# Kernel optimization log

Measured on AMD Instinct MI355X. Metric: run time of the kernel, lower is better.

The kernel has to match this reference:

```python
import jax, jax.numpy as jnp
import numpy as np
from jax import lax

B, C, H, W = 16, 3, 256, 256
K = 3          # lbp kernel size (odd)
POOL = 3       # avg pool size (odd so shapes are preserved)
Q = 8          # quant_len


def _build_lbp_kernel():
    mid = K // 2
    idx_pairs = [((0, 0), (K - 1, K - 1)), ((0, mid), (K - 1, mid)),
                 ((0, K - 1), (K - 1, 0)), ((mid, K - 1), (mid, 0))]
    ks = []
    for a, b in idx_pairs:
        for pos in (a, b):
            k = np.zeros((C, K, K), np.float32)
            k[:, mid, mid] = 1.0
            k[:, pos[0], pos[1]] = -1.0
            ks.append(k)
    return jnp.asarray(np.stack(ks))  # [8, C, K, K]

LBP_KERNEL = _build_lbp_kernel()
# cartesian_prod(arange(Q), arange(Q)) -> first coord slowest (row-major)
IDXS = jnp.asarray(np.stack(np.meshgrid(np.arange(Q), np.arange(Q), indexing='ij'), -1)
                   .reshape(Q * Q, 2).astype(np.float32))  # [64, 2]


def _forward(x, w_expand, b_expand, w_conv, b_conv, w_final, b_final, clamp_low, clamp_high):
    b = x.shape[0]
    # avg_pool2d(kernel=POOL, stride=1, pad=POOL//2, count_include_pad=True)
    p = POOL // 2
    xp = jnp.pad(x, ((0, 0), (0, 0), (p, p), (p, p)))
    x = lax.reduce_window(xp, 0.0, lax.add, (1, 1, POOL, POOL), (1, 1, 1, 1), 'VALID') / (POOL * POOL)
    # 8-channel LBP difference conv, 'same' padding
    x = lax.conv_general_dilated(x, LBP_KERNEL, (1, 1), ((K // 2, K // 2), (K // 2, K // 2)),
                                 dimension_numbers=('NCHW', 'OIHW', 'NCHW'))  # [B,8,H,W]
    x = jnp.clip(x, clamp_low[0], clamp_high[0])
    b4 = b * 4
    v = x.reshape(b4, 2, H * W)                    # pairwise channels
    mn = v.min(-1)                                 # [b4,2]
    mx = v.max(-1)
    lev = mn[..., None] + (mx - mn)[..., None] * (jnp.arange(Q, dtype=v.dtype) / Q)  # [b4,2,Q]
    hi = jnp.concatenate([lev[..., 1:], mx[..., None]], -1)                          # [b4,2,Q]
    vq = v[:, :, None, :]                                                            # [b4,2,1,HW]
    # keep value if lev[l] <= v <= hi[l], else 0 (values equal to a boundary land in both bins)
    masked = jnp.where((vq >= lev[..., None]) & (vq <= hi[..., None]), vq, 0.0)      # [b4,2,Q,HW]
    # joint weighted histogram: sum_p v0[p in bin i] * v1[p in bin j]
    hist = jnp.einsum('bip,bjp->bij', masked[:, 0], masked[:, 1])                    # [b4,Q,Q]
    hist = (hist / jnp.sum(hist)).reshape(b4, Q * Q)
    feats = jnp.concatenate([jnp.broadcast_to(IDXS, (b4, Q * Q, 2)), hist[..., None]], -1)  # [b4,64,3]
    f = feats.reshape(b, 4, Q * Q, 3).transpose(0, 3, 1, 2)                          # [B,3,4,64]
    y = jax.nn.leaky_relu(jnp.einsum('bchw,oc->bohw', f, w_expand) + b_expand[None, :, None, None])
    y = y.transpose(0, 2, 3, 1)                                                      # [B,4,64,56]
    # torch nearest interpolate: src = floor(dst * in / out)
    h_in, w_in = y.shape[-2], y.shape[-1]
    rows = (jnp.arange(H) * h_in) // H
    cols = (jnp.arange(W) * w_in) // W
    y = y[:, :, rows][:, :, :, cols]                                                 # [B,4,H,W]
    # layer_norm over last two dims, no affine
    mean = y.mean((-2, -1), keepdims=True)
    var = ((y - mean) ** 2).mean((-2, -1), keepdims=True)
    y = (y - mean) / jnp.sqrt(var + 1e-5)
    y = jax.nn.leaky_relu(jnp.einsum('bchw,oc->bohw', y, w_conv) + b_conv[None, :, None, None])
    y = lax.conv_general_dilated(y, w_final, (1, 1), ((1, 1), (1, 1)),
                                 dimension_numbers=('NCHW', 'OIHW', 'NCHW')) + b_final[None, :, None, None]
    return jax.nn.leaky_relu(y)                                                      # [B,1,H,W]


def setup_inputs() -> dict:
    key = jax.random.key(0)
    ks = jax.random.split(key, 7)
    return {
        'x': jax.random.normal(ks[0], (B, C, H, W), jnp.float32),
        'w_expand': jax.random.normal(ks[1], (56, 3), jnp.float32) * 0.1,
        'b_expand': jax.random.normal(ks[2], (56,), jnp.float32) * 0.1,
        'w_conv': jax.random.normal(ks[3], (16, 4), jnp.float32) * 0.1,
        'b_conv': jax.random.normal(ks[4], (16,), jnp.float32) * 0.1,
        'w_final': jax.random.normal(ks[5], (1, 16, 3, 3), jnp.float32) * 0.1,
        'b_final': jax.random.normal(ks[6], (1,), jnp.float32) * 0.1,
        'clamp_low': jnp.full((1,), -150.0, jnp.float32),
        'clamp_high': jnp.full((1,), 150.0, jnp.float32),
    }


def reference(x, w_expand, b_expand, w_conv, b_conv, w_final, b_final, clamp_low, clamp_high):
    return _forward(x, w_expand, b_expand, w_conv, b_conv, w_final, b_final, clamp_low, clamp_high)
```

## Files before the change

### kernel.cpp

```cpp
#include <hip/hip_runtime.h>
#include <math.h>

#define NB   16
#define HW   65536
#define NCHH 16

#define OFF_S    0
#define OFF_D    0
#define OFF_PH   1048576
#define OFF_PMN  1114112
#define OFF_PMX  1122304

__device__ __forceinline__ float leakyf(float v) { return v >= 0.f ? v : 0.01f * v; }

__global__ void __launch_bounds__(256) k_boxmm(const float* __restrict__ x,
                                               const float* __restrict__ clo,
                                               const float* __restrict__ chi,
                                               float* __restrict__ ws)
{
    __shared__ float inp[36][37];
    __shared__ float S[34][36];
    const int doy[8] = {-1, 1, -1, 1, -1, 1, 0, 0};
    const int dox[8] = {-1, 1,  0, 0,  1, -1, 1, -1};
    int b = blockIdx.z;
    int h0 = blockIdx.y * 32, w0 = blockIdx.x * 32;
    int tid = threadIdx.x;
    const float* xb = x + (size_t)b * 3 * HW;
    for (int i = tid; i < 36 * 36; i += 256) {
        int lh = i / 36, lw = i % 36;
        int gh = h0 - 2 + lh, gw = w0 - 2 + lw;
        float v = 0.f;
        if ((unsigned)gh < 256u && (unsigned)gw < 256u) {
            int p = gh * 256 + gw;
            v = xb[p] + xb[HW + p] + xb[2 * HW + p];
        }
        inp[lh][lw] = v;
    }
    __syncthreads();
    for (int i = tid; i < 34 * 34; i += 256) {
        int lh = i / 34, lw = i % 34;
        float s = 0.f;
        #pragma unroll
        for (int dy = 0; dy < 3; ++dy)
            #pragma unroll
            for (int dx = 0; dx < 3; ++dx)
                s += inp[lh + dy][lw + dx];
        S[lh][lw] = s / 9.0f;
    }
    __syncthreads();
    #pragma unroll
    for (int i = 0; i < 4; ++i) {
        int idx = i * 256 + tid;
        int r = idx >> 5, c = idx & 31;
        ws[OFF_S + b * HW + (h0 + r) * 256 + (w0 + c)] = S[r + 1][c + 1];
    }
    float lo = clo[0], hi = chi[0];
    float vmn[8], vmx[8];
    #pragma unroll
    for (int o = 0; o < 8; ++o) { vmn[o] = 3.4e38f; vmx[o] = -3.4e38f; }
    #pragma unroll
    for (int i = 0; i < 4; ++i) {
        int idx = i * 256 + tid;
        int r = idx >> 5, c = idx & 31;
        int gh = h0 + r, gw = w0 + c;
        float sc = S[r + 1][c + 1];
        #pragma unroll
        for (int o = 0; o < 8; ++o) {
            int nh = gh + doy[o], nw = gw + dox[o];
            float off = ((unsigned)nh < 256u && (unsigned)nw < 256u)
                        ? S[r + 1 + doy[o]][c + 1 + dox[o]] : 0.f;
            float v = fminf(fmaxf(sc - off, lo), hi);
            vmn[o] = fminf(vmn[o], v);
            vmx[o] = fmaxf(vmx[o], v);
        }
    }
    #pragma unroll
    for (int o = 0; o < 8; ++o) {
        #pragma unroll
        for (int m = 1; m < 64; m <<= 1) {
            vmn[o] = fminf(vmn[o], __shfl_xor(vmn[o], m));
            vmx[o] = fmaxf(vmx[o], __shfl_xor(vmx[o], m));
        }
    }
    __shared__ float smn[4][8], smx[4][8];
    int wid = tid >> 6, lane = tid & 63;
    if (lane == 0) {
        #pragma unroll
        for (int o = 0; o < 8; ++o) { smn[wid][o] = vmn[o]; smx[wid][o] = vmx[o]; }
    }
    __syncthreads();
    if (tid < 8) {
        int o = tid;
        int tile = blockIdx.y * 8 + blockIdx.x;
        float mn = fminf(fminf(smn[0][o], smn[1][o]), fminf(smn[2][o], smn[3][o]));
        float mx = fmaxf(fmaxf(smx[0][o], smx[1][o]), fmaxf(smx[2][o], smx[3][o]));
        ws[OFF_PMN + (b * 8 + o) * 64 + tile] = mn;
        ws[OFF_PMX + (b * 8 + o) * 64 + tile] = mx;
    }
}

__global__ void __launch_bounds__(256) k_hist_part(const float* __restrict__ clo,
                                                   const float* __restrict__ chi,
                                                   float* ws)
{
    __shared__ float lh[64 * 64];
    __shared__ float sred[4];
    const int doy[8] = {-1, 1, -1, 1, -1, 1, 0, 0};
    const int dox[8] = {-1, 1,  0, 0,  1, -1, 1, -1};
    int bg = blockIdx.x / NCHH;
    int ch = blockIdx.x % NCHH;
    int b = bg >> 2, g = bg & 3;
    int dy0 = doy[2 * g], dx0 = dox[2 * g];
    int dy1 = doy[2 * g + 1], dx1 = dox[2 * g + 1];
    int tid = threadIdx.x;
    int warp = tid >> 6, lane = tid & 63;
    {
        int c0 = (b * 8 + 2 * g) * 64, c1 = (b * 8 + 2 * g + 1) * 64;
        float v;
        if      (warp == 0) v = ws[OFF_PMN + c0 + lane];
        else if (warp == 1) v = ws[OFF_PMX + c0 + lane];
        else if (warp == 2) v = ws[OFF_PMN + c1 + lane];
        else                v = ws[OFF_PMX + c1 + lane];
        bool isMin = (warp & 1) == 0;
        #pragma unroll
        for (int m = 1; m < 64; m <<= 1) {
            float o = __shfl_xor(v, m);
            v = isMin ? fminf(v, o) : fmaxf(v, o);
        }
        if (lane == 0) sred[warp] = v;
    }
    for (int i = tid; i < 4096; i += 256) lh[i] = 0.f;
    __syncthreads();
    float mn0 = sred[0], mx0 = sred[1], mn1 = sred[2], mx1 = sred[3];
    float r0 = mx0 - mn0, r1 = mx1 - mn1;
    float lev0[8], lev1[8];
    #pragma unroll
    for (int q = 0; q < 8; ++q) {
        lev0[q] = __fadd_rn(mn0, __fmul_rn(r0, (float)q * 0.125f));
        lev1[q] = __fadd_rn(mn1, __fmul_rn(r1, (float)q * 0.125f));
    }
    const float* Sb = ws + OFF_S + b * HW;
    int col = tid & 63;
    float lo = clo[0], hi = chi[0];
    int base = ch * (HW / NCHH);
    #pragma unroll
    for (int it = 0; it < (HW / NCHH) / 256; ++it) {
        int p = base + it * 256 + tid;
        int h = p >> 8, w = p & 255;
        float off0 = 0.f, off1 = 0.f;
        int nh = h + dy0, nw = w + dx0;
        if ((unsigned)nh < 256u && (unsigned)nw < 256u) off0 = Sb[nh * 256 + nw];
        nh = h + dy1; nw = w + dx1;
        if ((unsigned)nh < 256u && (unsigned)nw < 256u) off1 = Sb[nh * 256 + nw];
        float sc = Sb[p];
        float v0 = fminf(fmaxf(sc - off0, lo), hi);
        float v1 = fminf(fmaxf(sc - off1, lo), hi);
        int i0 = 0, j0 = 0;
        bool ilo = false, jlo = false;
        #pragma unroll
        for (int k = 1; k < 8; ++k) {
            i0 += (v0 >= lev0[k]); ilo |= (v0 == lev0[k]);
            j0 += (v1 >= lev1[k]); jlo |= (v1 == lev1[k]);
        }
        float prod = v0 * v1;
        atomicAdd(&lh[(i0 * 8 + j0) * 64 + col], prod);
        if (ilo)        atomicAdd(&lh[((i0 - 1) * 8 + j0) * 64 + col], prod);
        if (jlo)        atomicAdd(&lh[(i0 * 8 + (j0 - 1)) * 64 + col], prod);
        if (ilo && jlo) atomicAdd(&lh[((i0 - 1) * 8 + (j0 - 1)) * 64 + col], prod);
    }
    __syncthreads();
    if (tid < 64) {
        int bin = tid;
        float s = 0.f;
        for (int c = 0; c < 64; ++c) s += lh[bin * 64 + ((c + bin) & 63)];
        ws[OFF_PH + blockIdx.x * 64 + bin] = s;
    }
}

__global__ void __launch_bounds__(256) k_fuse(const float* __restrict__ we,
                                              const float* __restrict__ be,
                                              const float* __restrict__ wc,
                                              const float* __restrict__ bc,
                                              const float* __restrict__ wf,
                                              float* ws)
{
    __shared__ float shY[4 * 3584];
    __shared__ float sh_hist[256];
    __shared__ float sh_red[256];
    __shared__ float sh_wf[144];
    __shared__ float sh_we[168];
    __shared__ float sh_be[56];
    __shared__ float sh_wc[64];
    __shared__ float sh_bc[16];
    __shared__ float sh_stat[8];
    __shared__ float sw[4][8];
    __shared__ float sh_tot;
    int b = blockIdx.x;
    int tid = threadIdx.x;

    {
        int g = tid >> 6, bin = tid & 63;
        float s = 0.f;
        #pragma unroll
        for (int c = 0; c < NCHH; ++c)
            s += ws[OFF_PH + ((b * 4 + g) * NCHH + c) * 64 + bin];
        sh_hist[tid] = s;
    }
    {
        const float4* ph4 = (const float4*)(ws + OFF_PH);
        float s = 0.f;
        for (int k = 0; k < 64; ++k) {
            float4 v = ph4[k * 256 + tid];
            s += v.x + v.y + v.z + v.w;
        }
        sh_red[tid] = s;
    }
    if (tid < 144) sh_wf[tid] = wf[tid];
    if (tid < 168) sh_we[tid] = we[tid];
    if (tid < 56)  sh_be[tid] = be[tid];
    if (tid < 64)  sh_wc[tid] = wc[tid];
    if (tid < 16)  sh_bc[tid] = bc[tid];
    __syncthreads();
    for (int k = 128; k > 0; k >>= 1) {
        if (tid < k) sh_red[tid] += sh_red[tid + k];
        __syncthreads();
    }
    if (tid == 0) sh_tot = sh_red[0];
    __syncthreads();
    float total = sh_tot;

    float ls[4] = {0.f, 0.f, 0.f, 0.f}, lss[4] = {0.f, 0.f, 0.f, 0.f};
    for (int it = 0; it < 56; ++it) {
        int g = it / 14;
        int rem = (it % 14) * 256 + tid;
        int q = rem / 56, o = rem % 56;
        float hv = sh_hist[g * 64 + q] / total;
        float y = sh_we[o * 3 + 0] * (float)(q >> 3)
                + sh_we[o * 3 + 1] * (float)(q & 7)
                + sh_we[o * 3 + 2] * hv + sh_be[o];
        y = leakyf(y);
        shY[g * 3584 + rem] = y;
        int cnt = ((32 * (o + 1) + 6) / 7) - ((32 * o + 6) / 7);
        float wgt = (float)(4 * cnt);
        ls[g]  += y * wgt;
        lss[g] += y * y * wgt;
    }
    #pragma unroll
    for (int g = 0; g < 4; ++g) {
        #pragma unroll
        for (int m = 1; m < 64; m <<= 1) {
            ls[g]  += __shfl_xor(ls[g], m);
            lss[g] += __shfl_xor(lss[g], m);
        }
    }
    int wid = tid >> 6, lane = tid & 63;
    if (lane == 0) {
        #pragma unroll
        for (int g = 0; g < 4; ++g) { sw[wid][g] = ls[g]; sw[wid][4 + g] = lss[g]; }
    }
    __syncthreads();
    if (tid < 4) {
        float m  = (sw[0][tid] + sw[1][tid] + sw[2][tid] + sw[3][tid]) / 65536.f;
        float sq = (sw[0][4 + tid] + sw[1][4 + tid] + sw[2][4 + tid] + sw[3][4 + tid]) / 65536.f;
        sh_stat[tid] = m;
        sh_stat[4 + tid] = 1.f / sqrtf(sq - m * m + 1e-5f);
    }
    __syncthreads();

    for (int it = 0; it < 14; ++it) {
        int rem = it * 256 + tid;
        float yn[4];
        #pragma unroll
        for (int g = 0; g < 4; ++g)
            yn[g] = (shY[g * 3584 + rem] - sh_stat[g]) * sh_stat[4 + g];
        float d[9] = {0.f, 0.f, 0.f, 0.f, 0.f, 0.f, 0.f, 0.f, 0.f};
        #pragma unroll
        for (int c = 0; c < 16; ++c) {
            float z = sh_bc[c];
            #pragma unroll
            for (int g = 0; g < 4; ++g) z += sh_wc[c * 4 + g] * yn[g];
            z = leakyf(z);
            #pragma unroll
            for (int t = 0; t < 9; ++t) d[t] += z * sh_wf[c * 9 + t];
        }
        #pragma unroll
        for (int t = 0; t < 9; ++t)
            ws[OFF_D + (b * 9 + t) * 3584 + rem] = d[t];
    }
}

__global__ void __launch_bounds__(256) k_final(const float* __restrict__ ws,
                                               const float* __restrict__ bf,
                                               float* __restrict__ out)
{
    int pix = blockIdx.x * 256 + threadIdx.x;
    int w = pix & 255, h = (pix >> 8) & 255, b = pix >> 16;
    const float* Db = ws + OFF_D + b * 9 * 3584;
    float acc = 0.f;
    #pragma unroll
    for (int kh = 0; kh < 3; ++kh) {
        int h2 = h + kh - 1;
        if ((unsigned)h2 > 255u) continue;
        int qr = h2 >> 2;
        #pragma unroll
        for (int kw = 0; kw < 3; ++kw) {
            int w2 = w + kw - 1;
            if ((unsigned)w2 > 255u) continue;
            int oc = (w2 * 7) >> 5;
            acc += Db[(kh * 3 + kw) * 3584 + qr * 56 + oc];
        }
    }
    out[pix] = leakyf(acc + bf[0]);
}

extern "C" void kernel_launch(void* const* d_in, const int* in_sizes, int n_in,
                              void* d_out, int out_size, void* d_ws, size_t ws_size,
                              hipStream_t stream)
{
    const float* x   = (const float*)d_in[0];
    const float* we  = (const float*)d_in[1];
    const float* be  = (const float*)d_in[2];
    const float* wc  = (const float*)d_in[3];
    const float* bc  = (const float*)d_in[4];
    const float* wf  = (const float*)d_in[5];
    const float* bfi = (const float*)d_in[6];
    const float* clo = (const float*)d_in[7];
    const float* chi = (const float*)d_in[8];
    float* out = (float*)d_out;
    float* ws  = (float*)d_ws;

    k_boxmm<<<dim3(8, 8, NB), 256, 0, stream>>>(x, clo, chi, ws);
    k_hist_part<<<64 * NCHH, 256, 0, stream>>>(clo, chi, ws);
    k_fuse<<<NB, 256, 0, stream>>>(we, be, wc, bc, wf, ws);
    k_final<<<4096, 256, 0, stream>>>(ws, bfi, out);
}
```

Before: 153.2 us.

## Split fuse kernel across slices, precompute histogram totals, vectorize final output

k_fuse now launches 7 blocks per batch instead of one. Each block recomputes the cheap expand/statistics step and handles only 2 of the 14 output iterations, which drops the large shared Y buffer. Per-block histogram totals are reduced inside k_hist_part with wave shuffles, so k_fuse no longer re-reads the full partial histogram array to get the normaliser. k_final computes 4 pixels per thread and writes them with a float4 store. The cost is redundant stats work in every k_fuse block, traded for more parallelism in what was a 16-block serial bottleneck.

```diff
diff --git a/kernel.cpp b/kernel.cpp
--- a/kernel.cpp
+++ b/kernel.cpp
@@ -10,6 +10,7 @@
 #define OFF_PH   1048576
 #define OFF_PMN  1114112
 #define OFF_PMX  1122304
+#define OFF_PT   1130496
 
 __device__ __forceinline__ float leakyf(float v) { return v >= 0.f ? v : 0.01f * v; }
 
@@ -174,6 +175,10 @@
         float s = 0.f;
         for (int c = 0; c < 64; ++c) s += lh[bin * 64 + ((c + bin) & 63)];
         ws[OFF_PH + blockIdx.x * 64 + bin] = s;
+        float t = s;
+        #pragma unroll
+        for (int m = 1; m < 64; m <<= 1) t += __shfl_xor(t, m);
+        if (bin == 0) ws[OFF_PT + blockIdx.x] = t;
     }
 }
 
@@ -184,7 +189,6 @@
                                               const float* __restrict__ wf,
                                               float* ws)
 {
-    __shared__ float shY[4 * 3584];
     __shared__ float sh_hist[256];
     __shared__ float sh_red[256];
     __shared__ float sh_wf[144];
@@ -195,7 +199,8 @@
     __shared__ float sh_stat[8];
     __shared__ float sw[4][8];
     __shared__ float sh_tot;
-    int b = blockIdx.x;
+    int b     = blockIdx.x / 7;
+    int slice = blockIdx.x % 7;
     int tid = threadIdx.x;
 
     {
@@ -207,12 +212,8 @@
         sh_hist[tid] = s;
     }
     {
-        const float4* ph4 = (const float4*)(ws + OFF_PH);
-        float s = 0.f;
-        for (int k = 0; k < 64; ++k) {
-            float4 v = ph4[k * 256 + tid];
-            s += v.x + v.y + v.z + v.w;
-        }
+        float s = ws[OFF_PT + tid] + ws[OFF_PT + 256 + tid]
+                + ws[OFF_PT + 512 + tid] + ws[OFF_PT + 768 + tid];
         sh_red[tid] = s;
     }
     if (tid < 144) sh_wf[tid] = wf[tid];
@@ -230,20 +231,20 @@
     float total = sh_tot;
 
     float ls[4] = {0.f, 0.f, 0.f, 0.f}, lss[4] = {0.f, 0.f, 0.f, 0.f};
-    for (int it = 0; it < 56; ++it) {
-        int g = it / 14;
-        int rem = (it % 14) * 256 + tid;
+    for (int it = 0; it < 14; ++it) {
+        int rem = it * 256 + tid;
         int q = rem / 56, o = rem % 56;
-        float hv = sh_hist[g * 64 + q] / total;
-        float y = sh_we[o * 3 + 0] * (float)(q >> 3)
-                + sh_we[o * 3 + 1] * (float)(q & 7)
-                + sh_we[o * 3 + 2] * hv + sh_be[o];
-        y = leakyf(y);
-        shY[g * 3584 + rem] = y;
+        float base = sh_we[o * 3 + 0] * (float)(q >> 3)
+                   + sh_we[o * 3 + 1] * (float)(q & 7) + sh_be[o];
+        float w2 = sh_we[o * 3 + 2];
         int cnt = ((32 * (o + 1) + 6) / 7) - ((32 * o + 6) / 7);
         float wgt = (float)(4 * cnt);
-        ls[g]  += y * wgt;
-        lss[g] += y * y * wgt;
+        #pragma unroll
+        for (int g = 0; g < 4; ++g) {
+            float y = leakyf(base + w2 * (sh_hist[g * 64 + q] / total));
+            ls[g]  += y * wgt;
+            lss[g] += y * y * wgt;
+        }
     }
     #pragma unroll
     for (int g = 0; g < 4; ++g) {
@@ -267,12 +268,18 @@
     }
     __syncthreads();
 
-    for (int it = 0; it < 14; ++it) {
+    for (int it = slice * 2; it < slice * 2 + 2; ++it) {
         int rem = it * 256 + tid;
+        int q = rem / 56, o = rem % 56;
+        float base = sh_we[o * 3 + 0] * (float)(q >> 3)
+                   + sh_we[o * 3 + 1] * (float)(q & 7) + sh_be[o];
+        float w2 = sh_we[o * 3 + 2];
         float yn[4];
         #pragma unroll
-        for (int g = 0; g < 4; ++g)
-            yn[g] = (shY[g * 3584 + rem] - sh_stat[g]) * sh_stat[4 + g];
+        for (int g = 0; g < 4; ++g) {
+            float y = leakyf(base + w2 * (sh_hist[g * 64 + q] / total));
+            yn[g] = (y - sh_stat[g]) * sh_stat[4 + g];
+        }
         float d[9] = {0.f, 0.f, 0.f, 0.f, 0.f, 0.f, 0.f, 0.f, 0.f};
         #pragma unroll
         for (int c = 0; c < 16; ++c) {
@@ -293,10 +300,13 @@
                                                const float* __restrict__ bf,
                                                float* __restrict__ out)
 {
-    int pix = blockIdx.x * 256 + threadIdx.x;
-    int w = pix & 255, h = (pix >> 8) & 255, b = pix >> 16;
+    int t4 = blockIdx.x * 256 + threadIdx.x;
+    int b = t4 >> 14;
+    int rem = t4 & 16383;
+    int h = rem >> 6, w0 = (rem & 63) * 4;
     const float* Db = ws + OFF_D + b * 9 * 3584;
-    float acc = 0.f;
+    float bias = bf[0];
+    float acc[4] = {bias, bias, bias, bias};
     #pragma unroll
     for (int kh = 0; kh < 3; ++kh) {
         int h2 = h + kh - 1;
@@ -304,13 +314,18 @@
         int qr = h2 >> 2;
         #pragma unroll
         for (int kw = 0; kw < 3; ++kw) {
-            int w2 = w + kw - 1;
-            if ((unsigned)w2 > 255u) continue;
-            int oc = (w2 * 7) >> 5;
-            acc += Db[(kh * 3 + kw) * 3584 + qr * 56 + oc];
-        }
-    }
-    out[pix] = leakyf(acc + bf[0]);
+            const float* Dt = Db + (kh * 3 + kw) * 3584 + qr * 56;
+            #pragma unroll
+            for (int j = 0; j < 4; ++j) {
+                int w2 = w0 + j + kw - 1;
+                if ((unsigned)w2 <= 255u) acc[j] += Dt[(w2 * 7) >> 5];
+            }
+        }
+    }
+    float4 o4;
+    o4.x = leakyf(acc[0]); o4.y = leakyf(acc[1]);
+    o4.z = leakyf(acc[2]); o4.w = leakyf(acc[3]);
+    ((float4*)out)[t4] = o4;
 }
 
 extern "C" void kernel_launch(void* const* d_in, const int* in_sizes, int n_in,
@@ -331,6 +346,6 @@
 
     k_boxmm<<<dim3(8, 8, NB), 256, 0, stream>>>(x, clo, chi, ws);
     k_hist_part<<<64 * NCHH, 256, 0, stream>>>(clo, chi, ws);
-    k_fuse<<<NB, 256, 0, stream>>>(we, be, wc, bc, wf, ws);
-    k_final<<<4096, 256, 0, stream>>>(ws, bfi, out);
-}
+    k_fuse<<<NB * 7, 256, 0, stream>>>(we, be, wc, bc, wf, ws);
+    k_final<<<1024, 256, 0, stream>>>(ws, bfi, out);
+}
```

Result: faster. 131.5 us (-14.2%).
